# Performance work log

Measured on AMD Instinct MI355X. Metric: run time of the kernel, lower is better.

Reference implementation:

```python
import jax, jax.numpy as jnp
import numpy as np

B, SEQ, NVAR, DM, K = 2, 512, 64, 128, 2
SCALE = DM ** -0.5  # ScaledDotProductAttention scale, lsa=False so constant


def _period_branch(x4, Wel, bel, Wq, bq, Wk, bk, Wv, bv, Wo, bo, period):
    # x4: [B, DM(time), NVAR, DM(dim)] -- output of start_embed
    pad = (-DM) % period
    pn = (DM + pad) // period  # period_num
    xp = jnp.pad(x4, ((0, 0), (0, pad), (0, 0), (0, 0)))
    # torch .unfold(dim=1, size=period, step=period) -> [B, pn, NVAR, DM, period]
    xw = xp.reshape(B, pn, period, NVAR, DM).transpose(0, 1, 3, 4, 2)
    # emb_linear over the d_model (dim) axis
    xw = jnp.einsum('bqndl,ed->bqnel', xw, Wel) + bel[None, None, None, :, None]
    # -> [B, NVAR, dim, pn, period] then flatten to conv1d layout [bn, dim, L]
    X = xw.transpose(0, 2, 3, 1, 4).reshape(B * NVAR, DM, pn * period)
    # 1x1 Conv1d QKV projections over the channel (dim) axis
    q = jnp.einsum('bdl,ed->bel', X, Wq) + bq[None, :, None]
    k = jnp.einsum('bdl,ed->bel', X, Wk) + bk[None, :, None]
    v = jnp.einsum('bdl,ed->bel', X, Wv) + bv[None, :, None]
    q_s = q.reshape(B * NVAR, DM, pn, period).transpose(0, 1, 3, 2)  # [bn,dim,pl,pn]
    k_s = k.reshape(B * NVAR, DM, pn, period)                         # [bn,dim,pn,pl]
    v_s = v.reshape(B * NVAR, DM, pn, period).transpose(0, 1, 3, 2)  # [bn,dim,pl,pn]
    attn = jax.nn.softmax(jnp.einsum('bdip,bdpj->bdij', q_s, k_s) * SCALE, axis=-1)
    o = jnp.einsum('bdij,bdjp->bdip', attn, v_s)  # [bn, dim, period, pn]
    o = o.reshape(B * NVAR, DM, period * pn)[:, :, :DM]  # truncate to n_heads=DM
    return o @ Wo.T + bo  # to_out Linear(n_heads, n_heads), dropout eval-mode


def reference(x, W_emb, b_emb, W_start, b_start, Wel, bel, Wq, bq, Wk, bk, Wv, bv, Wo, bo, f1, f2):
    # inverted embedding: Linear(seq_len->d_model) over time, then permute -> [B, DM, NVAR]
    xe = (jnp.einsum('bsn,sd->bnd', x, W_emb) + b_emb).transpose(0, 2, 1)
    # FFT_for_Period amplitudes; top-k frequency indices f1,f2 are static (host-side in torch)
    amp = jnp.abs(jnp.fft.rfft(xe, axis=1)).mean(-1)  # [B, DM//2+1]
    pw = jax.nn.softmax(jnp.stack([amp[:, f1], amp[:, f2]], -1), axis=-1)  # [B, K]
    # start_embed: Linear(1 -> d_model) -> [B, DM, NVAR, DM]
    x4 = xe[..., None] * W_start + b_start
    outs = [_period_branch(x4, Wel, bel, Wq, bq, Wk, bk, Wv, bv, Wo, bo, DM // f)
            for f in (f1, f2)]
    res = jnp.stack(outs, -1)                      # [B*NVAR, DM, DM, K]
    pw_b = jnp.repeat(pw, NVAR, axis=0)            # [B*NVAR, K] (b-major order matches reshape)
    out = (res * pw_b[:, None, None, :]).sum(-1)
    return out.reshape(B, NVAR, DM, DM)


def setup_inputs() -> dict:
    key = jax.random.key(0)
    ks = jax.random.split(key, 16)
    s = 0.02
    d = {
        'x': jax.random.normal(ks[0], (B, SEQ, NVAR), jnp.float32),
        'W_emb': jax.random.normal(ks[1], (SEQ, DM), jnp.float32) * s,
        'b_emb': jax.random.normal(ks[2], (DM,), jnp.float32) * s,
        'W_start': jax.random.normal(ks[3], (DM,), jnp.float32) * s,
        'b_start': jax.random.normal(ks[4], (DM,), jnp.float32) * s,
        'Wel': jax.random.normal(ks[5], (DM, DM), jnp.float32) * s,
        'bel': jax.random.normal(ks[6], (DM,), jnp.float32) * s,
        'Wq': jax.random.normal(ks[7], (DM, DM), jnp.float32) * s,
        'bq': jax.random.normal(ks[8], (DM,), jnp.float32) * s,
        'Wk': jax.random.normal(ks[9], (DM, DM), jnp.float32) * s,
        'bk': jax.random.normal(ks[10], (DM,), jnp.float32) * s,
        'Wv': jax.random.normal(ks[11], (DM, DM), jnp.float32) * s,
        'bv': jax.random.normal(ks[12], (DM,), jnp.float32) * s,
        'Wo': jax.random.normal(ks[13], (DM, DM), jnp.float32) * s,
        'bo': jax.random.normal(ks[14], (DM,), jnp.float32) * s,
    }
    # host-side FFT period detection, mirroring torch's .detach().cpu().numpy() topk
    xe = np.einsum('bsn,sd->bnd', np.asarray(d['x']), np.asarray(d['W_emb'])) + np.asarray(d['b_emb'])
    xe = xe.transpose(0, 2, 1)  # [B, DM, NVAR]
    fl = np.abs(np.fft.rfft(xe, axis=1)).mean(0).mean(-1)
    fl[0] = 0.0
    top = np.argsort(-fl, kind='stable')[:K]
    d['f1'] = int(top[0])
    d['f2'] = int(top[1])
    return d
```

## Files before the change

kernel.cpp:

```cpp
#include <hip/hip_runtime.h>

#define DMD 128
#define NV 64
#define BB 2
#define SQ 512
#define NBN 128
#define ASCALE 0.08838834764831845f
#define L2E 1.4426950408889634f
#define CSC (ASCALE * L2E)

#define WS_XE  0
#define WS_VEC (WS_XE + NBN*DMD)
#define WS_OB  (WS_VEC + 9*DMD)
#define WS_AMP (WS_OB + NBN*DMD*DMD)

__global__ __launch_bounds__(512) void k_xe(const float* __restrict__ x,
                                            const float* __restrict__ W_emb,
                                            const float* __restrict__ b_emb,
                                            const int* __restrict__ f1p,
                                            const int* __restrict__ f2p,
                                            const float* __restrict__ Wel, const float* __restrict__ bel,
                                            const float* __restrict__ W_start, const float* __restrict__ b_start,
                                            const float* __restrict__ Wq, const float* __restrict__ bq,
                                            const float* __restrict__ Wk, const float* __restrict__ bk,
                                            const float* __restrict__ Wv, const float* __restrict__ bv,
                                            float* __restrict__ ws) {
    int blk = blockIdx.x;
    int tid = threadIdx.x;
    __shared__ float xsh[SQ];
    __shared__ float part[3][DMD];
    __shared__ float red[2][4];
    __shared__ __align__(16) float A[DMD], C[DMD], BL[DMD];

    if (blk < NBN) {
        int bn = blk, b = bn >> 6, n = bn & 63;
        int t = tid & 127, sc = tid >> 7;
        xsh[tid] = x[(b * SQ + tid) * NV + n];
        __syncthreads();
        float acc = 0.f;
        const float* W = W_emb + (sc * 128) * DMD + t;
#pragma unroll 8
        for (int s = 0; s < 128; ++s) acc = fmaf(xsh[sc * 128 + s], W[s * DMD], acc);
        if (sc) part[sc - 1][t] = acc;
        __syncthreads();
        if (sc == 0) {
            float r = acc + part[0][t] + part[1][t] + part[2][t] + b_emb[t];
            ws[WS_XE + bn * DMD + t] = r;
            int f1v = f1p[0], f2v = f2p[0];
            float angA = (float)((f1v * t) & 127) * 0.04908738521234052f;
            float angB = (float)((f2v * t) & 127) * 0.04908738521234052f;
            float v0 = r * cosf(angA), v1 = r * sinf(angA);
            float v2 = r * cosf(angB), v3 = r * sinf(angB);
#pragma unroll
            for (int off = 32; off > 0; off >>= 1) {
                v0 += __shfl_xor(v0, off); v1 += __shfl_xor(v1, off);
                v2 += __shfl_xor(v2, off); v3 += __shfl_xor(v3, off);
            }
            if ((tid & 63) == 0) {
                int w = tid >> 6;
                red[w][0] = v0; red[w][1] = v1; red[w][2] = v2; red[w][3] = v3;
            }
        }
        __syncthreads();
        if (tid == 0) {
            float re0 = red[0][0] + red[1][0], im0 = red[0][1] + red[1][1];
            float re1 = red[0][2] + red[1][2], im1 = red[0][3] + red[1][3];
            ws[WS_AMP + bn * 2 + 0] = sqrtf(re0 * re0 + im0 * im0);
            ws[WS_AMP + bn * 2 + 1] = sqrtf(re1 * re1 + im1 * im1);
        }
    } else {
        int e = tid;
        if (tid < 128) {
            float a = 0.f, c = 0.f;
            const float4* We4 = reinterpret_cast<const float4*>(Wel + e * DMD);
            const float4* Ws4 = reinterpret_cast<const float4*>(W_start);
            const float4* Bs4 = reinterpret_cast<const float4*>(b_start);
#pragma unroll 8
            for (int d4 = 0; d4 < 32; ++d4) {
                float4 w = We4[d4], s4 = Ws4[d4], t4 = Bs4[d4];
                a = fmaf(w.x, s4.x, fmaf(w.y, s4.y, fmaf(w.z, s4.z, fmaf(w.w, s4.w, a))));
                c = fmaf(w.x, t4.x, fmaf(w.y, t4.y, fmaf(w.z, t4.z, fmaf(w.w, t4.w, c))));
            }
            A[e] = a;
            C[e] = c + bel[e];
            BL[e] = bel[e];
        }
        __syncthreads();
        if (tid < 128) {
            float aq = 0, cq = 0, pq = 0, ak = 0, ck = 0, pk = 0, av = 0, cv = 0, pv = 0;
            const float4* Wq4 = reinterpret_cast<const float4*>(Wq + e * DMD);
            const float4* Wk4 = reinterpret_cast<const float4*>(Wk + e * DMD);
            const float4* Wv4 = reinterpret_cast<const float4*>(Wv + e * DMD);
            const float4* A4 = reinterpret_cast<const float4*>(A);
            const float4* C4 = reinterpret_cast<const float4*>(C);
            const float4* B4 = reinterpret_cast<const float4*>(BL);
#pragma unroll 4
            for (int d4 = 0; d4 < 32; ++d4) {
                float4 Ad = A4[d4], Cd = C4[d4], Bd = B4[d4];
                float4 wq = Wq4[d4], wk = Wk4[d4], wv = Wv4[d4];
                aq = fmaf(wq.x, Ad.x, fmaf(wq.y, Ad.y, fmaf(wq.z, Ad.z, fmaf(wq.w, Ad.w, aq))));
                cq = fmaf(wq.x, Cd.x, fmaf(wq.y, Cd.y, fmaf(wq.z, Cd.z, fmaf(wq.w, Cd.w, cq))));
                pq = fmaf(wq.x, Bd.x, fmaf(wq.y, Bd.y, fmaf(wq.z, Bd.z, fmaf(wq.w, Bd.w, pq))));
                ak = fmaf(wk.x, Ad.x, fmaf(wk.y, Ad.y, fmaf(wk.z, Ad.z, fmaf(wk.w, Ad.w, ak))));
                ck = fmaf(wk.x, Cd.x, fmaf(wk.y, Cd.y, fmaf(wk.z, Cd.z, fmaf(wk.w, Cd.w, ck))));
                pk = fmaf(wk.x, Bd.x, fmaf(wk.y, Bd.y, fmaf(wk.z, Bd.z, fmaf(wk.w, Bd.w, pk))));
                av = fmaf(wv.x, Ad.x, fmaf(wv.y, Ad.y, fmaf(wv.z, Ad.z, fmaf(wv.w, Ad.w, av))));
                cv = fmaf(wv.x, Cd.x, fmaf(wv.y, Cd.y, fmaf(wv.z, Cd.z, fmaf(wv.w, Cd.w, cv))));
                pv = fmaf(wv.x, Bd.x, fmaf(wv.y, Bd.y, fmaf(wv.z, Bd.z, fmaf(wv.w, Bd.w, pv))));
            }
            float* V = ws + WS_VEC;
            V[0 * DMD + e] = aq; V[1 * DMD + e] = cq + bq[e]; V[2 * DMD + e] = pq + bq[e];
            V[3 * DMD + e] = ak; V[4 * DMD + e] = ck + bk[e]; V[5 * DMD + e] = pk + bk[e];
            V[6 * DMD + e] = av; V[7 * DMD + e] = cv + bv[e]; V[8 * DMD + e] = pv + bv[e];
        }
    }
}


__device__ __forceinline__ void attn_rank1(const float (*Vsh)[4],
                                           const float* xs, float* __restrict__ ob,
                                           int rowbase, int tid) {
    float xi = xs[tid];
    float t[4], l[4], ax[4];
#pragma unroll
    for (int k = 0; k < 4; ++k) {
        float Aq = Vsh[0][k], Cq = Vsh[1][k], Ak = Vsh[3][k];
        t[k] = CSC * fmaf(xi, Aq, Cq) * Ak;
        l[k] = 0.f; ax[k] = 0.f;
    }
#pragma unroll 4
    for (int j = 0; j < DMD; ++j) {
        float xj = xs[j];
#pragma unroll
        for (int k = 0; k < 4; ++k) {
            float ev = exp2f(t[k] * xj);
            l[k] += ev;
            ax[k] = fmaf(ev, xj, ax[k]);
        }
    }
#pragma unroll
    for (int k = 0; k < 4; ++k) {
        float Av = Vsh[6][k], Cv = Vsh[7][k];
        ob[rowbase + k * DMD + tid] = fmaf(Av, ax[k] / l[k], Cv);
    }
}

template<int PP, int NP, int EB>
__device__ __forceinline__ void attn_pow2(const float (*Vsh)[4],
                                          const float* xs, float* __restrict__ ob,
                                          int rowbase, int tid) {
    const int UH = PP / 4;
    int lane4 = tid & 3, i0 = tid >> 2, jb = lane4 * UH;

    float xq[NP][UH], U2[UH];
#pragma unroll
    for (int u = 0; u < UH; ++u) {
        int j = jb + u;
        float s = 0.f;
#pragma unroll
        for (int q = 0; q < NP; ++q) { float xv = xs[q * PP + j]; xq[q][u] = xv; s += xv; }
        U2[u] = s;
    }
    const int NREP = (PP == 64) ? 2 : 1;
#pragma unroll
    for (int rep = 0; rep < NREP; ++rep) {
        int i = i0 + rep * 32;
        float G2[UH];
#pragma unroll
        for (int u = 0; u < UH; ++u) G2[u] = 0.f;
#pragma unroll
        for (int q = 0; q < NP; ++q) {
            float xi = xs[q * PP + i];
#pragma unroll
            for (int u = 0; u < UH; ++u) G2[u] = fmaf(xi, xq[q][u], G2[u]);
        }
#pragma unroll
        for (int eg = 0; eg < 4; eg += EB) {
            float d1[EB], d2[EB], l[EB];
            float accq[NP][EB];
#pragma unroll
            for (int k = 0; k < EB; ++k) {
                float t = CSC * Vsh[3][eg + k];
                d1[k] = t * Vsh[0][eg + k];
                d2[k] = t * Vsh[1][eg + k];
                l[k] = 0.f;
#pragma unroll
                for (int q = 0; q < NP; ++q) accq[q][k] = 0.f;
            }
#pragma unroll
            for (int u = 0; u < UH; ++u) {
                float gg = G2[u], uu = U2[u];
                float ev[EB];
#pragma unroll
                for (int k = 0; k < EB; ++k) ev[k] = exp2f(fmaf(d1[k], gg, d2[k] * uu));
#pragma unroll
                for (int k = 0; k < EB; ++k) {
                    l[k] += ev[k];
#pragma unroll
                    for (int q = 0; q < NP; ++q) accq[q][k] = fmaf(ev[k], xq[q][u], accq[q][k]);
                }
            }
#pragma unroll
            for (int k = 0; k < EB; ++k) { l[k] += __shfl_xor(l[k], 1); l[k] += __shfl_xor(l[k], 2); }
#pragma unroll
            for (int q = 0; q < NP; ++q)
#pragma unroll
                for (int k = 0; k < EB; ++k) {
                    accq[q][k] += __shfl_xor(accq[q][k], 1);
                    accq[q][k] += __shfl_xor(accq[q][k], 2);
                }
            if (lane4 == 0) {
#pragma unroll
                for (int k = 0; k < EB; ++k) {
                    float li = 1.f / l[k];
                    float Av = Vsh[6][eg + k], Cv = Vsh[7][eg + k];
#pragma unroll
                    for (int q = 0; q < NP; ++q) {
                        ob[rowbase + (eg + k) * DMD + i * NP + q] = fmaf(Av, accq[q][k] * li, Cv);
                    }
                }
            }
        }
    }
}

template<int UB>
__device__ __forceinline__ void attn_small(
    int P, int pn, int r, int Prows,
    const float (*Vsh)[4], const float* xs, const float* U, const float* xt,
    float* W, float* __restrict__ ob, int rowbase, int tid)
{
    int GP = P + 1;
    int tot = Prows * P;
    unsigned mP = (4096u + (unsigned)P - 1u) / (unsigned)P;
    unsigned mpn = (4096u + (unsigned)pn - 1u) / (unsigned)pn;

    bool v0 = (tid < tot);
    int i0 = (int)(((unsigned)tid * mP) >> 12);
    int j0 = tid - i0 * P;
    bool A0 = (i0 < r), c0 = (j0 < r);
    float xtj0 = xt[j0], Uj0 = U[j0];
    float xti0 = A0 ? xt[i0] : 0.f;
    float g0 = 0.f;
    for (int p = 0; p < pn - 1; ++p) g0 = fmaf(xs[p * P + i0], xs[p * P + j0], g0);
    float Gx0 = (A0 && c0) ? fmaf(xti0, xtj0, g0) : g0;
    float Ux0 = (A0 && c0) ? Uj0 + xtj0 : Uj0;
    float Xw0 = (!A0 && c0) ? xtj0 : 0.f;
    float mw0 = c0 ? 1.f : 0.f;
    int wa0 = i0 * GP + j0;

    int idx1 = tid + 128;
    bool v1 = (idx1 < tot);
    int idx1c = v1 ? idx1 : 0;
    int i1 = (int)(((unsigned)idx1c * mP) >> 12);
    int j1 = idx1c - i1 * P;
    bool A1 = (i1 < r), c1 = (j1 < r);
    float xtj1 = xt[j1], Uj1 = U[j1];
    float xti1 = A1 ? xt[i1] : 0.f;
    float g1 = 0.f;
    for (int p = 0; p < pn - 1; ++p) g1 = fmaf(xs[p * P + i1], xs[p * P + j1], g1);
    float Gx1 = (A1 && c1) ? fmaf(xti1, xtj1, g1) : g1;
    float Ux1 = (A1 && c1) ? Uj1 + xtj1 : Uj1;
    float Xw1 = (!A1 && c1) ? xtj1 : 0.f;
    float mw1 = c1 ? 1.f : 0.f;
    int wa1 = i1 * GP + j1;

    int i2 = (int)(((unsigned)tid * mpn) >> 12);
    int p2 = tid - i2 * pn;
    bool lastp = (p2 == pn - 1);
    int row2 = i2 * GP;
    float xsr[UB];
#pragma unroll
    for (int j = 0; j < UB; ++j) {
        int idx = p2 * P + j;
        xsr[j] = (j < P && idx < DMD) ? xs[idx] : 0.f;
    }

    float s[4][2];
#pragma unroll
    for (int ec = 0; ec < 4; ++ec) {
        float Aq = Vsh[0][ec], Cq = Vsh[1][ec], Pq = Vsh[2][ec];
        float Ak = Vsh[3][ec], Ck = Vsh[4][ec], Pk = Vsh[5][ec];
        float t = CSC * Ak;
        float d1 = t * Aq, d2 = t * Cq, d3 = t * Pq;
        float ckpk = CSC * (Ck - Pk);
        float aS0 = A0 ? fmaf(Aq, xti0, Cq) : Pq;
        s[ec][0] = fmaf(d1, Gx0, fmaf(d2, Ux0, fmaf(d3, Xw0, (ckpk * aS0) * mw0)));
        float aS1 = A1 ? fmaf(Aq, xti1, Cq) : Pq;
        s[ec][1] = fmaf(d1, Gx1, fmaf(d2, Ux1, fmaf(d3, Xw1, (ckpk * aS1) * mw1)));
    }
#pragma unroll
    for (int ec = 0; ec < 4; ++ec) { s[ec][0] = exp2f(s[ec][0]); s[ec][1] = exp2f(s[ec][1]); }
#pragma unroll
    for (int ec = 0; ec < 4; ++ec) {
        if (v0) W[ec * 288 + wa0] = s[ec][0];
        if (v1) W[ec * 288 + wa1] = s[ec][1];
    }
    __syncthreads();

#pragma unroll
    for (int ec = 0; ec < 4; ++ec) {
        float Av = Vsh[6][ec], Cv = Vsh[7][ec], Pv = Vsh[8][ec];
        float l = 0.f, wr = 0.f, ax = 0.f;
#pragma unroll
        for (int j = 0; j < UB; ++j) {
            float w = W[ec * 288 + row2 + ((j < P) ? j : 0)];
            w = (j < P) ? w : 0.f;
            l += w;
            wr += (j < r) ? w : 0.f;
            ax = fmaf(w, xsr[j], ax);
        }
        float li = 1.f / l;
        float o;
        if (lastp) { float sl = wr * li; o = fmaf(Av, ax * li, fmaf(Cv, sl, Pv * (1.f - sl))); }
        else       o = fmaf(Av, ax * li, Cv);
        ob[rowbase + ec * DMD + tid] = o;
    }
}

template<int UH, int NP>
__device__ __forceinline__ void attn_midA(
    int P, int pn, int r, int Prows,
    const float (*Vsh)[4], const float* xs, const float* U,
    const float* xt, float* __restrict__ ob, int rowbase, int tid)
{
    int lane4 = tid & 3;
    int i0 = tid >> 2;
    int jb = lane4 * UH;

    float Ur[UH], xtr[UH], xq0[UH], xq1[UH];
#pragma unroll
    for (int u = 0; u < UH; ++u) {
        int j = jb + u, jc = (j < P) ? j : 0;
        Ur[u] = U[jc];
        xtr[u] = xt[jc];
        xq0[u] = (j < DMD) ? xs[j] : 0.f;
        int i1x = P + j;
        xq1[u] = (i1x < DMD) ? xs[i1x] : 0.f;
    }
    int nrep = (Prows > 32) ? 2 : 1;
    for (int rep = 0; rep < nrep; ++rep) {
        int i = i0 + rep * 32;
        bool rowact = (i < Prows);
        int ic = rowact ? i : 0;
        float xtic = xt[ic];
        bool rowvalid = (ic < r);
        float g[UH];
#pragma unroll
        for (int u = 0; u < UH; ++u) g[u] = 0.f;
        for (int p = 0; p < pn - 1; ++p) {
            float xi = xs[p * P + ic];
#pragma unroll
            for (int u = 0; u < UH; ++u) {
                int j = jb + u, jc = (j < P) ? j : 0;
                g[u] = fmaf(xi, xs[p * P + jc], g[u]);
            }
        }
        for (int ec = 0; ec < 4; ++ec) {
            float Aq = Vsh[0][ec], Cq = Vsh[1][ec], Pq = Vsh[2][ec];
            float Ak = Vsh[3][ec], Ck = Vsh[4][ec], Pk = Vsh[5][ec];
            float Av = Vsh[6][ec], Cv = Vsh[7][ec], Pv = Vsh[8][ec];
            float c1 = CSC * Aq * Ak, c3 = CSC * Cq * Ak;
            float asi = CSC * (rowvalid ? fmaf(xtic, Aq, Cq) : Pq);

            float l0 = 0.f, l1 = 0.f, w0 = 0.f, w1 = 0.f;
            float accq[NP];
#pragma unroll
            for (int q = 0; q < NP; ++q) accq[q] = 0.f;
#pragma unroll
            for (int u = 0; u < UH; ++u) {
                int j = jb + u;
                float bK = (j < r) ? fmaf(xtr[u], Ak, Ck) : Pk;
                float S = fmaf(asi, bK, fmaf(c3, Ur[u], c1 * g[u]));
                float ev = exp2f(S);
                ev = (j < P) ? ev : 0.f;
                if (u & 1) l1 += ev; else l0 += ev;
                float evr = (j < r) ? ev : 0.f;
                if (u & 1) w1 += evr; else w0 += evr;
                accq[0] = fmaf(ev, xq0[u], accq[0]);
                if (NP >= 2) accq[1] = fmaf(ev, xq1[u], accq[1]);
#pragma unroll
                for (int q = 2; q < NP; ++q) {
                    int idx = q * P + j;
                    float xv = (idx < DMD) ? xs[idx] : 0.f;
                    accq[q] = fmaf(ev, xv, accq[q]);
                }
            }
            float l = l0 + l1, wr = w0 + w1;
            l += __shfl_xor(l, 1);  l += __shfl_xor(l, 2);
            wr += __shfl_xor(wr, 1); wr += __shfl_xor(wr, 2);
#pragma unroll
            for (int q = 0; q < NP; ++q) {
                if (q < pn) {
                    accq[q] += __shfl_xor(accq[q], 1);
                    accq[q] += __shfl_xor(accq[q], 2);
                }
            }
            if (lane4 == 0 && rowact) {
                float li = 1.f / l;
#pragma unroll
                for (int q = 0; q < NP; ++q) {
                    if (q < pn) {
                        int mo = i * pn + q;
                        if (mo < DMD) {
                            float o;
                            if (q == pn - 1) {
                                float sl = wr * li;
                                o = fmaf(Av, accq[q] * li, fmaf(Cv, sl, Pv * (1.f - sl)));
                            } else {
                                o = fmaf(Av, accq[q] * li, Cv);
                            }
                            ob[rowbase + ec * DMD + mo] = o;
                        }
                    }
                }
            }
        }
    }
}

__global__ __launch_bounds__(128) void k_attn(const int* __restrict__ f1p,
                                              const int* __restrict__ f2p,
                                              float* __restrict__ ws,
                                              float* __restrict__ outb) {
    int bn = blockIdx.y;
    int e0 = blockIdx.x * 4;
    int br = blockIdx.z;
    int tid = threadIdx.x;

    __shared__ float xs[DMD], U[64], xt[64];
    __shared__ float Vsh[9][4];
    __shared__ float W[4 * 288];

    xs[tid] = ws[WS_XE + bn * DMD + tid];
    if (tid < 36) Vsh[tid >> 2][tid & 3] = ws[WS_VEC + (tid >> 2) * DMD + e0 + (tid & 3)];
    int f = br ? f2p[0] : f1p[0];
    float* ob = br ? outb : (ws + WS_OB);
    int rowbase = (bn * DMD + e0) * DMD;
    __syncthreads();

    int P = DMD / f;
    int pn = (DMD + P - 1) / P;
    int r = DMD - (pn - 1) * P;
    int Prows = (DMD + pn - 1) / pn;

    if (P == DMD) {
        attn_rank1(Vsh, xs, ob, rowbase, tid);
        return;
    }
    if (tid < P) {
        float s = 0.f;
        for (int p = 0; p < pn - 1; ++p) s += xs[p * P + tid];
        U[tid] = s;
        xt[tid] = (tid < r) ? xs[(pn - 1) * P + tid] : 0.f;
    }
    __syncthreads();

    if (P <= 4)       attn_small<4>(P, pn, r, Prows, Vsh, xs, U, xt, W, ob, rowbase, tid);
    else if (P <= 8)  attn_small<8>(P, pn, r, Prows, Vsh, xs, U, xt, W, ob, rowbase, tid);
    else if (P <= 16) attn_small<16>(P, pn, r, Prows, Vsh, xs, U, xt, W, ob, rowbase, tid);
    else if (P == 64) attn_pow2<64, 2, 2>(Vsh, xs, ob, rowbase, tid);
    else if (P == 32) attn_pow2<32, 4, 4>(Vsh, xs, ob, rowbase, tid);
    else if (P > 32)  attn_midA<16, 4>(P, pn, r, Prows, Vsh, xs, U, xt, ob, rowbase, tid);
    else              attn_midA<8, 8>(P, pn, r, Prows, Vsh, xs, U, xt, ob, rowbase, tid);
}

__global__ __launch_bounds__(256) void k_out(const float* __restrict__ Wo,
                                             const float* __restrict__ bo,
                                             const float* __restrict__ ws,
                                             float* __restrict__ out) {
    int blk = blockIdx.x;
    int bn0 = (blk >> 2) * 2;
    int e0  = (blk & 3) * 32;
    int b = bn0 >> 6;
    int tid = threadIdx.x;
    __shared__ __align__(16) float WTc[32 * 132];
    __shared__ __align__(16) float oT[2][32][36];
    __shared__ float pwsh[2];
    int hg = tid & 31, eg = tid >> 5, h0 = hg * 4;

    if (tid < 64) {
        float a0 = ws[WS_AMP + (b * NV + tid) * 2 + 0];
        float a1 = ws[WS_AMP + (b * NV + tid) * 2 + 1];
#pragma unroll
        for (int off = 32; off > 0; off >>= 1) {
            a0 += __shfl_down(a0, off);
            a1 += __shfl_down(a1, off);
        }
        if (tid == 0) {
            a0 *= (1.0f / NV); a1 *= (1.0f / NV);
            float m = fmaxf(a0, a1);
            float e0v = expf(a0 - m), e1v = expf(a1 - m);
            float inv = 1.0f / (e0v + e1v);
            pwsh[0] = e0v * inv;
            pwsh[1] = e1v * inv;
        }
    }
    __syncthreads();
    float pw0 = pwsh[0], pw1 = pwsh[1];

    float acc[2][4][4];
#pragma unroll
    for (int a = 0; a < 2; ++a)
#pragma unroll
        for (int c = 0; c < 4; ++c)
#pragma unroll
            for (int d = 0; d < 4; ++d) acc[a][c][d] = 0.f;

    for (int mc = 0; mc < 4; ++mc) {
        int m0 = mc * 32;
        __syncthreads();
        for (int idx = tid; idx < 4096; idx += 256) {
            int h = idx >> 5, mm = idx & 31;
            WTc[mm * 132 + h] = Wo[h * DMD + m0 + mm];
        }
        for (int idx = tid; idx < 2048; idx += 256) {
            int bnl = idx >> 10, rem = idx & 1023, e = rem >> 5, mm = rem & 31;
            int gi = ((bn0 + bnl) * DMD + e0 + e) * DMD + m0 + mm;
            oT[bnl][mm][e] = fmaf(pw0, ws[WS_OB + gi], pw1 * out[gi]);
        }
        __syncthreads();
#pragma unroll 4
        for (int mm = 0; mm < 32; ++mm) {
            const float4 wv = *reinterpret_cast<const float4*>(&WTc[mm * 132 + h0]);
            const float4 q0 = *reinterpret_cast<const float4*>(&oT[0][mm][eg * 4]);
            const float4 q1 = *reinterpret_cast<const float4*>(&oT[1][mm][eg * 4]);
            float ae[2][4] = {{q0.x, q0.y, q0.z, q0.w}, {q1.x, q1.y, q1.z, q1.w}};
#pragma unroll
            for (int bnl = 0; bnl < 2; ++bnl) {
#pragma unroll
                for (int el = 0; el < 4; ++el) {
                    float a = ae[bnl][el];
                    acc[bnl][el][0] = fmaf(a, wv.x, acc[bnl][el][0]);
                    acc[bnl][el][1] = fmaf(a, wv.y, acc[bnl][el][1]);
                    acc[bnl][el][2] = fmaf(a, wv.z, acc[bnl][el][2]);
                    acc[bnl][el][3] = fmaf(a, wv.w, acc[bnl][el][3]);
                }
            }
        }
    }
    const float4 bov = *reinterpret_cast<const float4*>(&bo[h0]);
#pragma unroll
    for (int bnl = 0; bnl < 2; ++bnl) {
#pragma unroll
        for (int el = 0; el < 4; ++el) {
            float4 res = { acc[bnl][el][0] + bov.x, acc[bnl][el][1] + bov.y,
                           acc[bnl][el][2] + bov.z, acc[bnl][el][3] + bov.w };
            int e = e0 + eg * 4 + el;
            *reinterpret_cast<float4*>(&out[((bn0 + bnl) * DMD + e) * DMD + h0]) = res;
        }
    }
}

extern "C" void kernel_launch(void* const* d_in, const int* in_sizes, int n_in,
                              void* d_out, int out_size, void* d_ws, size_t ws_size,
                              hipStream_t stream) {
    const float* x       = (const float*)d_in[0];
    const float* W_emb   = (const float*)d_in[1];
    const float* b_emb   = (const float*)d_in[2];
    const float* W_start = (const float*)d_in[3];
    const float* b_start = (const float*)d_in[4];
    const float* Wel     = (const float*)d_in[5];
    const float* bel     = (const float*)d_in[6];
    const float* Wq      = (const float*)d_in[7];
    const float* bq      = (const float*)d_in[8];
    const float* Wk      = (const float*)d_in[9];
    const float* bk      = (const float*)d_in[10];
    const float* Wv      = (const float*)d_in[11];
    const float* bv      = (const float*)d_in[12];
    const float* Wo      = (const float*)d_in[13];
    const float* bo      = (const float*)d_in[14];
    const int*   f1p     = (const int*)d_in[15];
    const int*   f2p     = (const int*)d_in[16];
    float* ws  = (float*)d_ws;
    float* out = (float*)d_out;

    k_xe<<<NBN + 1, 512, 0, stream>>>(x, W_emb, b_emb, f1p, f2p,
                                      Wel, bel, W_start, b_start,
                                      Wq, bq, Wk, bk, Wv, bv, ws);
    k_attn<<<dim3(32, NBN, 2), 128, 0, stream>>>(f1p, f2p, ws, out);
    k_out<<<256, 256, 0, stream>>>(Wo, bo, ws, out);
}
```

Baseline: 81.01 us.

## Precompute Gram sums in k_xe and split k_out per bn row

For small periods (P<=16), k_xe now computes the partial Gram dot products over x_e once per (bn, branch) and stores them in a new workspace region. attn_small loads them instead of recomputing them in every one of the 32 e-blocks. Separately, k_out now handles one bn per block instead of two, doubling its grid to 512 blocks to raise parallelism. The cost is reloading Wo tiles for every block and adding extra work to k_xe.

```diff
diff --git a/kernel.cpp b/kernel.cpp
--- a/kernel.cpp
+++ b/kernel.cpp
@@ -13,6 +13,7 @@
 #define WS_VEC (WS_XE + NBN*DMD)
 #define WS_OB  (WS_VEC + 9*DMD)
 #define WS_AMP (WS_OB + NBN*DMD*DMD)
+#define WS_G   (WS_AMP + NBN*2)
 
 __global__ __launch_bounds__(512) void k_xe(const float* __restrict__ x,
                                             const float* __restrict__ W_emb,
@@ -30,11 +31,13 @@
     __shared__ float xsh[SQ];
     __shared__ float part[3][DMD];
     __shared__ float red[2][4];
+    __shared__ float xe_sh[DMD];
     __shared__ __align__(16) float A[DMD], C[DMD], BL[DMD];
 
     if (blk < NBN) {
         int bn = blk, b = bn >> 6, n = bn & 63;
         int t = tid & 127, sc = tid >> 7;
+        int f1v = f1p[0], f2v = f2p[0];
         xsh[tid] = x[(b * SQ + tid) * NV + n];
         __syncthreads();
         float acc = 0.f;
@@ -46,7 +49,7 @@
         if (sc == 0) {
             float r = acc + part[0][t] + part[1][t] + part[2][t] + b_emb[t];
             ws[WS_XE + bn * DMD + t] = r;
-            int f1v = f1p[0], f2v = f2p[0];
+            xe_sh[t] = r;
             float angA = (float)((f1v * t) & 127) * 0.04908738521234052f;
             float angB = (float)((f2v * t) & 127) * 0.04908738521234052f;
             float v0 = r * cosf(angA), v1 = r * sinf(angA);
@@ -67,6 +70,25 @@
             float re1 = red[0][2] + red[1][2], im1 = red[0][3] + red[1][3];
             ws[WS_AMP + bn * 2 + 0] = sqrtf(re0 * re0 + im0 * im0);
             ws[WS_AMP + bn * 2 + 1] = sqrtf(re1 * re1 + im1 * im1);
+        }
+        {
+            int br = tid >> 8;
+            int entry = tid & 255;
+            int f = br ? f2v : f1v;
+            int P = DMD / f;
+            if (P <= 16) {
+                int pn = (DMD + P - 1) / P;
+                int Prows = (DMD + pn - 1) / pn;
+                int tot = Prows * P;
+                if (entry < tot) {
+                    int i = entry / P;
+                    int j = entry - i * P;
+                    float g = 0.f;
+                    for (int p = 0; p < pn - 1; ++p)
+                        g = fmaf(xe_sh[p * P + i], xe_sh[p * P + j], g);
+                    ws[WS_G + (bn * 2 + br) * 288 + i * (P + 1) + j] = g;
+                }
+            }
         }
     } else {
         int e = tid;
@@ -228,7 +250,7 @@
 __device__ __forceinline__ void attn_small(
     int P, int pn, int r, int Prows,
     const float (*Vsh)[4], const float* xs, const float* U, const float* xt,
-    float* W, float* __restrict__ ob, int rowbase, int tid)
+    const float* __restrict__ Gb, float* W, float* __restrict__ ob, int rowbase, int tid)
 {
     int GP = P + 1;
     int tot = Prows * P;
@@ -238,32 +260,30 @@
     bool v0 = (tid < tot);
     int i0 = (int)(((unsigned)tid * mP) >> 12);
     int j0 = tid - i0 * P;
+    int wa0 = i0 * GP + j0;
+    float g0 = Gb[wa0];
     bool A0 = (i0 < r), c0 = (j0 < r);
     float xtj0 = xt[j0], Uj0 = U[j0];
     float xti0 = A0 ? xt[i0] : 0.f;
-    float g0 = 0.f;
-    for (int p = 0; p < pn - 1; ++p) g0 = fmaf(xs[p * P + i0], xs[p * P + j0], g0);
     float Gx0 = (A0 && c0) ? fmaf(xti0, xtj0, g0) : g0;
     float Ux0 = (A0 && c0) ? Uj0 + xtj0 : Uj0;
     float Xw0 = (!A0 && c0) ? xtj0 : 0.f;
     float mw0 = c0 ? 1.f : 0.f;
-    int wa0 = i0 * GP + j0;
 
     int idx1 = tid + 128;
     bool v1 = (idx1 < tot);
     int idx1c = v1 ? idx1 : 0;
     int i1 = (int)(((unsigned)idx1c * mP) >> 12);
     int j1 = idx1c - i1 * P;
+    int wa1 = i1 * GP + j1;
+    float g1 = Gb[wa1];
     bool A1 = (i1 < r), c1 = (j1 < r);
     float xtj1 = xt[j1], Uj1 = U[j1];
     float xti1 = A1 ? xt[i1] : 0.f;
-    float g1 = 0.f;
-    for (int p = 0; p < pn - 1; ++p) g1 = fmaf(xs[p * P + i1], xs[p * P + j1], g1);
     float Gx1 = (A1 && c1) ? fmaf(xti1, xtj1, g1) : g1;
     float Ux1 = (A1 && c1) ? Uj1 + xtj1 : Uj1;
     float Xw1 = (!A1 && c1) ? xtj1 : 0.f;
     float mw1 = c1 ? 1.f : 0.f;
-    int wa1 = i1 * GP + j1;
 
     int i2 = (int)(((unsigned)tid * mpn) >> 12);
     int p2 = tid - i2 * pn;
@@ -436,6 +456,7 @@
     if (tid < 36) Vsh[tid >> 2][tid & 3] = ws[WS_VEC + (tid >> 2) * DMD + e0 + (tid & 3)];
     int f = br ? f2p[0] : f1p[0];
     float* ob = br ? outb : (ws + WS_OB);
+    const float* Gb = ws + WS_G + (bn * 2 + br) * 288;
     int rowbase = (bn * DMD + e0) * DMD;
     __syncthreads();
 
@@ -456,9 +477,9 @@
     }
     __syncthreads();
 
-    if (P <= 4)       attn_small<4>(P, pn, r, Prows, Vsh, xs, U, xt, W, ob, rowbase, tid);
-    else if (P <= 8)  attn_small<8>(P, pn, r, Prows, Vsh, xs, U, xt, W, ob, rowbase, tid);
-    else if (P <= 16) attn_small<16>(P, pn, r, Prows, Vsh, xs, U, xt, W, ob, rowbase, tid);
+    if (P <= 4)       attn_small<4>(P, pn, r, Prows, Vsh, xs, U, xt, Gb, W, ob, rowbase, tid);
+    else if (P <= 8)  attn_small<8>(P, pn, r, Prows, Vsh, xs, U, xt, Gb, W, ob, rowbase, tid);
+    else if (P <= 16) attn_small<16>(P, pn, r, Prows, Vsh, xs, U, xt, Gb, W, ob, rowbase, tid);
     else if (P == 64) attn_pow2<64, 2, 2>(Vsh, xs, ob, rowbase, tid);
     else if (P == 32) attn_pow2<32, 4, 4>(Vsh, xs, ob, rowbase, tid);
     else if (P > 32)  attn_midA<16, 4>(P, pn, r, Prows, Vsh, xs, U, xt, ob, rowbase, tid);
@@ -470,12 +491,12 @@
                                              const float* __restrict__ ws,
                                              float* __restrict__ out) {
     int blk = blockIdx.x;
-    int bn0 = (blk >> 2) * 2;
-    int e0  = (blk & 3) * 32;
-    int b = bn0 >> 6;
+    int bn = blk >> 2;
+    int e0 = (blk & 3) * 32;
+    int b = bn >> 6;
     int tid = threadIdx.x;
     __shared__ __align__(16) float WTc[32 * 132];
-    __shared__ __align__(16) float oT[2][32][36];
+    __shared__ __align__(16) float oT[32][36];
     __shared__ float pwsh[2];
     int hg = tid & 31, eg = tid >> 5, h0 = hg * 4;
 
@@ -499,13 +520,11 @@
     __syncthreads();
     float pw0 = pwsh[0], pw1 = pwsh[1];
 
-    float acc[2][4][4];
-#pragma unroll
-    for (int a = 0; a < 2; ++a)
-#pragma unroll
-        for (int c = 0; c < 4; ++c)
-#pragma unroll
-            for (int d = 0; d < 4; ++d) acc[a][c][d] = 0.f;
+    float acc[4][4];
+#pragma unroll
+    for (int c = 0; c < 4; ++c)
+#pragma unroll
+        for (int d = 0; d < 4; ++d) acc[c][d] = 0.f;
 
     for (int mc = 0; mc < 4; ++mc) {
         int m0 = mc * 32;
@@ -514,41 +533,34 @@
             int h = idx >> 5, mm = idx & 31;
             WTc[mm * 132 + h] = Wo[h * DMD + m0 + mm];
         }
-        for (int idx = tid; idx < 2048; idx += 256) {
-            int bnl = idx >> 10, rem = idx & 1023, e = rem >> 5, mm = rem & 31;
-            int gi = ((bn0 + bnl) * DMD + e0 + e) * DMD + m0 + mm;
-            oT[bnl][mm][e] = fmaf(pw0, ws[WS_OB + gi], pw1 * out[gi]);
+        for (int idx = tid; idx < 1024; idx += 256) {
+            int e = idx >> 5, mm = idx & 31;
+            int gi = (bn * DMD + e0 + e) * DMD + m0 + mm;
+            oT[mm][e] = fmaf(pw0, ws[WS_OB + gi], pw1 * out[gi]);
         }
         __syncthreads();
 #pragma unroll 4
         for (int mm = 0; mm < 32; ++mm) {
             const float4 wv = *reinterpret_cast<const float4*>(&WTc[mm * 132 + h0]);
-            const float4 q0 = *reinterpret_cast<const float4*>(&oT[0][mm][eg * 4]);
-            const float4 q1 = *reinterpret_cast<const float4*>(&oT[1][mm][eg * 4]);
-            float ae[2][4] = {{q0.x, q0.y, q0.z, q0.w}, {q1.x, q1.y, q1.z, q1.w}};
-#pragma unroll
-            for (int bnl = 0; bnl < 2; ++bnl) {
-#pragma unroll
-                for (int el = 0; el < 4; ++el) {
-                    float a = ae[bnl][el];
-                    acc[bnl][el][0] = fmaf(a, wv.x, acc[bnl][el][0]);
-                    acc[bnl][el][1] = fmaf(a, wv.y, acc[bnl][el][1]);
-                    acc[bnl][el][2] = fmaf(a, wv.z, acc[bnl][el][2]);
-                    acc[bnl][el][3] = fmaf(a, wv.w, acc[bnl][el][3]);
-                }
+            const float4 q0 = *reinterpret_cast<const float4*>(&oT[mm][eg * 4]);
+            float ae[4] = {q0.x, q0.y, q0.z, q0.w};
+#pragma unroll
+            for (int el = 0; el < 4; ++el) {
+                float a = ae[el];
+                acc[el][0] = fmaf(a, wv.x, acc[el][0]);
+                acc[el][1] = fmaf(a, wv.y, acc[el][1]);
+                acc[el][2] = fmaf(a, wv.z, acc[el][2]);
+                acc[el][3] = fmaf(a, wv.w, acc[el][3]);
             }
         }
     }
     const float4 bov = *reinterpret_cast<const float4*>(&bo[h0]);
 #pragma unroll
-    for (int bnl = 0; bnl < 2; ++bnl) {
-#pragma unroll
-        for (int el = 0; el < 4; ++el) {
-            float4 res = { acc[bnl][el][0] + bov.x, acc[bnl][el][1] + bov.y,
-                           acc[bnl][el][2] + bov.z, acc[bnl][el][3] + bov.w };
-            int e = e0 + eg * 4 + el;
-            *reinterpret_cast<float4*>(&out[((bn0 + bnl) * DMD + e) * DMD + h0]) = res;
-        }
+    for (int el = 0; el < 4; ++el) {
+        float4 res = { acc[el][0] + bov.x, acc[el][1] + bov.y,
+                       acc[el][2] + bov.z, acc[el][3] + bov.w };
+        int e = e0 + eg * 4 + el;
+        *reinterpret_cast<float4*>(&out[(bn * DMD + e) * DMD + h0]) = res;
     }
 }
 
@@ -579,5 +591,5 @@
                                       Wel, bel, W_start, b_start,
                                       Wq, bq, Wk, bk, Wv, bv, ws);
     k_attn<<<dim3(32, NBN, 2), 128, 0, stream>>>(f1p, f2p, ws, out);
-    k_out<<<256, 256, 0, stream>>>(Wo, bo, ws, out);
-}
+    k_out<<<512, 256, 0, stream>>>(Wo, bo, ws, out);
+}
```

Result: faster. 74.22 us (median of 2 runs) (-8.4%).
